# Optimization experiments

Hardware: AMD Instinct MI355X
Metric: run time of the kernel (lower is better)

Reference implementation:

```python
import jax, jax.numpy as jnp
import numpy as np
from jax import lax

EPS = 1e-5

def _conv1d(x, w, b):
    # x: [B,C,L], w: [O,I,K], valid padding, stride 1
    y = lax.conv_general_dilated(x, w, window_strides=(1,), padding='VALID',
                                 dimension_numbers=('NCH', 'OIH', 'NCH'))
    return y + b[None, :, None]

def setup_inputs() -> dict:
    key = jax.random.key(0)
    ks = jax.random.split(key, 7)
    B, L, C = 16, 4096, 512
    x = jax.random.normal(ks[0], (B, L, C), dtype=jnp.float32)
    fan3 = 1.0 / np.sqrt(C * 3)
    fan1 = 1.0 / np.sqrt(C * 1)
    w_down = jax.random.uniform(ks[1], (C, C, 3), jnp.float32, -fan3, fan3)
    b_down = jax.random.uniform(ks[2], (C,), jnp.float32, -fan3, fan3)
    w_pad = jax.random.uniform(ks[3], (C, C, 1), jnp.float32, -fan1, fan1)
    b_pad = jax.random.uniform(ks[4], (C,), jnp.float32, -fan1, fan1)
    gamma = jnp.ones((C,), jnp.float32)
    beta = jnp.zeros((C,), jnp.float32)
    return {"x": x, "w_down": w_down, "b_down": b_down,
            "w_pad": w_pad, "b_pad": b_pad, "gamma": gamma, "beta": beta}

def reference(x, w_down, b_down, w_pad, b_pad, gamma, beta):
    # d == 2 branch of ConvLayer
    B, L, C = x.shape

    def branch(xs):  # xs: [B, L//2, C]
        xt = jnp.transpose(xs, (0, 2, 1))                 # [B,C,L/2]
        p1 = _conv1d(xt, w_down, b_down)                  # [B,C,L/2-2]
        p2 = _conv1d(xt[:, :, :2], w_pad, b_pad)          # [B,C,2]
        return jnp.concatenate([p1, p2], axis=2)          # [B,C,L/2]

    x1_p = branch(x[:, 0::2, :])
    x2_p = branch(x[:, 1::2, :])
    # interleave: even positions from x1_p, odd from x2_p
    x_p = jnp.stack([x1_p, x2_p], axis=3).reshape(B, C, L)

    # BatchNorm1d in training mode: batch stats over (batch, length)
    mean = jnp.mean(x_p, axis=(0, 2), keepdims=True)
    var = jnp.var(x_p, axis=(0, 2), keepdims=True)
    xn = (x_p - mean) * lax.rsqrt(var + EPS)
    xn = xn * gamma[None, :, None] + beta[None, :, None]

    y = jax.nn.elu(xn)                                    # dropout = identity (eval)
    y = y + jnp.transpose(x, (0, 2, 1))                   # residual [B,C,L]

    # MaxPool1d(kernel=3, stride=2, padding=1)
    yp = jnp.pad(y, ((0, 0), (0, 0), (1, 1)), constant_values=-jnp.inf)
    pooled = lax.reduce_window(yp, -jnp.inf, lax.max, (1, 1, 3), (1, 1, 2), 'VALID')
    return jnp.transpose(pooled, (0, 2, 1))               # [B, L//2, C]
```

## Files before the change

kernel.cpp:

```cpp
#include <hip/hip_runtime.h>
#include <hip/hip_bf16.h>
#include <math.h>

typedef __bf16 bf16;
typedef __bf16 bf16x8 __attribute__((ext_vector_type(8)));
typedef float floatx4 __attribute__((ext_vector_type(4)));

#define GAS __attribute__((address_space(1)))
#define LAS __attribute__((address_space(3)))

static constexpr int B_ = 16, L_ = 4096, C_ = 512;
static constexpr int M_ = B_ * L_;
static constexpr int K_ = 3 * C_;

__global__ void prep(const float* __restrict__ x, bf16* __restrict__ xb,
                     const float* __restrict__ wd, bf16* __restrict__ wr,
                     const float* __restrict__ wp, const float* __restrict__ bp,
                     bf16* __restrict__ xp, float* __restrict__ sums) {
    __shared__ float xrow[C_];
    if (blockIdx.x < 2048) {
        for (int u = blockIdx.x; u < 19456; u += 2048) {
            if (u < 16384) {
                const size_t i = ((size_t)u * 256 + threadIdx.x) * 8;
                floatx4 a = *(const floatx4*)(x + i);
                floatx4 b = *(const floatx4*)(x + i + 4);
                bf16x8 o;
#pragma unroll
                for (int j = 0; j < 4; ++j) { o[j] = (bf16)a[j]; o[4 + j] = (bf16)b[j]; }
                *(bf16x8*)(xb + i) = o;
            } else {
                int idx = (u - 16384) * 256 + threadIdx.x;
                int o   = idx / K_;
                int rem = idx - o * K_;
                int kk  = rem >> 9;
                int i   = rem & 511;
                wr[idx] = (bf16)wd[o * K_ + i * 3 + kk];
            }
        }
    } else {
        const int bid = blockIdx.x - 2048;
        const int b = bid >> 2;
        const int j = bid & 3;
        for (int i = threadIdx.x; i < C_; i += 256)
            xrow[i] = x[(size_t)(b * L_ + j) * C_ + i];
        __syncthreads();
        for (int c = threadIdx.x; c < C_; c += 256) {
            const float* w = wp + (size_t)c * C_;
            float acc = 0.f;
#pragma unroll 4
            for (int i = 0; i < C_; i += 4) {
                floatx4 wv = *(const floatx4*)(w + i);
#pragma unroll
                for (int u = 0; u < 4; ++u) acc += wv[u] * xrow[i + u];
            }
            const float v = acc + bp[c];
            xp[(size_t)(b * L_ + 4092 + j) * C_ + c] = (bf16)v;
            atomicAdd(&sums[c], v);
            atomicAdd(&sums[C_ + c], v * v);
        }
    }
}

__global__ __launch_bounds__(512, 2) void gemm_conv(
    const bf16* __restrict__ x, const bf16* __restrict__ wr,
    const float* __restrict__ bd, bf16* __restrict__ xp, float* __restrict__ sums)
{
    __shared__ bf16 As[2 * 256 * 64];
    __shared__ bf16 Bs[2 * 256 * 64];

    const int tid = threadIdx.x;
    const int u   = blockIdx.x;
    const int mb  = (u & 7) + 8 * (u >> 4);
    const int nb  = (u >> 3) & 1;
    const int m0  = mb * 256;
    const int n0  = nb * 256;

    const int wave = tid >> 6;
    const int lane = tid & 63;
    const int wm = wave & 1;
    const int wn = wave >> 1;
    const int tm = lane & 15;
    const int quad = lane >> 4;

    floatx4 acc[2][4][2][2];
#pragma unroll
    for (int a = 0; a < 2; ++a)
#pragma unroll
        for (int b = 0; b < 4; ++b)
#pragma unroll
            for (int c = 0; c < 2; ++c)
#pragma unroll
                for (int d = 0; d < 2; ++d) acc[a][b][c][d] = floatx4{0.f, 0.f, 0.f, 0.f};

    const int r0  = tid >> 3;
    const int c0s = (tid & 7) ^ (r0 & 7);

    auto stageA = [&](int t, int eta) {
        if (t >= 24) return;
        const int kk = t >> 3, i0 = (t & 7) << 6;
        bf16* dst = As + (t & 1) * 16384 + eta * 8192 + tid * 8;
        int sr0 = m0 + eta * 128 + r0 + 2 * kk;      if (sr0 > M_ - 1) sr0 = M_ - 1;
        int sr1 = m0 + eta * 128 + r0 + 64 + 2 * kk; if (sr1 > M_ - 1) sr1 = M_ - 1;
        __builtin_amdgcn_global_load_lds((const GAS void*)(x + (size_t)sr0 * C_ + i0 + c0s * 8),
                                         (LAS void*)dst, 16, 0, 0);
        __builtin_amdgcn_global_load_lds((const GAS void*)(x + (size_t)sr1 * C_ + i0 + c0s * 8),
                                         (LAS void*)(dst + 4096), 16, 0, 0);
    };
    auto stageB = [&](int t, int eta) {
        if (t >= 24) return;
        const int kk = t >> 3, i0 = (t & 7) << 6;
        bf16* dst = Bs + (t & 1) * 16384 + eta * 8192 + tid * 8;
        const bf16* s0 = wr + (size_t)(n0 + eta * 128 + r0) * K_ + kk * C_ + i0 + c0s * 8;
        __builtin_amdgcn_global_load_lds((const GAS void*)s0, (LAS void*)dst, 16, 0, 0);
        __builtin_amdgcn_global_load_lds((const GAS void*)(s0 + (size_t)64 * K_),
                                         (LAS void*)(dst + 4096), 16, 0, 0);
    };

    const int xo0 = (quad ^ (tm & 7)) << 3;
    const int xo1 = ((4 + quad) ^ (tm & 7)) << 3;

    bf16x8 af[4][2];
    bf16x8 bfr[2][2][2];

    stageA(0, 0); stageB(0, 0); stageB(0, 1); stageA(0, 1);
    stageA(1, 0); stageB(1, 0); stageB(1, 1); stageA(1, 1);
    asm volatile("s_waitcnt vmcnt(8)" ::: "memory");
    asm volatile("s_barrier" ::: "memory");
#pragma unroll
    for (int mi = 0; mi < 4; ++mi) {
        const bf16* p = As + (wm * 64 + mi * 16 + tm) * 64;
        af[mi][0] = *(const bf16x8*)(p + xo0);
        af[mi][1] = *(const bf16x8*)(p + xo1);
    }
#pragma unroll
    for (int ni = 0; ni < 2; ++ni) {
        const bf16* p = Bs + (wn * 32 + ni * 16 + tm) * 64;
        bfr[0][ni][0] = *(const bf16x8*)(p + xo0);
        bfr[0][ni][1] = *(const bf16x8*)(p + xo1);
    }

#pragma unroll 2
    for (int t = 0; t < 24; ++t) {
        const bf16* Ab  = As + (t & 1) * 16384;
        const bf16* Bb  = Bs + (t & 1) * 16384;
        const bf16* AbN = As + ((t + 1) & 1) * 16384;
        const bf16* BbN = Bs + ((t + 1) & 1) * 16384;

        asm volatile("s_waitcnt lgkmcnt(0)" ::: "memory");
        __builtin_amdgcn_sched_barrier(0);
        __builtin_amdgcn_s_setprio(1);
#pragma unroll
        for (int kh = 0; kh < 2; ++kh)
#pragma unroll
            for (int mi = 0; mi < 4; ++mi)
#pragma unroll
                for (int ni = 0; ni < 2; ++ni)
                    acc[0][mi][0][ni] = __builtin_amdgcn_mfma_f32_16x16x32_bf16(
                        af[mi][kh], bfr[0][ni][kh], acc[0][mi][0][ni], 0, 0, 0);
        __builtin_amdgcn_s_setprio(0);
#pragma unroll
        for (int ni = 0; ni < 2; ++ni) {
            const bf16* p = Bb + (128 + wn * 32 + ni * 16 + tm) * 64;
            bfr[1][ni][0] = *(const bf16x8*)(p + xo0);
            bfr[1][ni][1] = *(const bf16x8*)(p + xo1);
        }
        asm volatile("s_barrier" ::: "memory");

        asm volatile("s_waitcnt lgkmcnt(0)" ::: "memory");
        __builtin_amdgcn_sched_barrier(0);
        __builtin_amdgcn_s_setprio(1);
#pragma unroll
        for (int kh = 0; kh < 2; ++kh)
#pragma unroll
            for (int mi = 0; mi < 4; ++mi)
#pragma unroll
                for (int ni = 0; ni < 2; ++ni)
                    acc[0][mi][1][ni] = __builtin_amdgcn_mfma_f32_16x16x32_bf16(
                        af[mi][kh], bfr[1][ni][kh], acc[0][mi][1][ni], 0, 0, 0);
        __builtin_amdgcn_s_setprio(0);
#pragma unroll
        for (int mi = 0; mi < 4; ++mi) {
            const bf16* p = Ab + (128 + wm * 64 + mi * 16 + tm) * 64;
            af[mi][0] = *(const bf16x8*)(p + xo0);
            af[mi][1] = *(const bf16x8*)(p + xo1);
        }
        stageA(t + 2, 0);
        stageB(t + 2, 0);
        asm volatile("s_barrier" ::: "memory");

        asm volatile("s_waitcnt lgkmcnt(0)" ::: "memory");
        __builtin_amdgcn_sched_barrier(0);
        __builtin_amdgcn_s_setprio(1);
#pragma unroll
        for (int kh = 0; kh < 2; ++kh)
#pragma unroll
            for (int mi = 0; mi < 4; ++mi)
#pragma unroll
                for (int ni = 0; ni < 2; ++ni)
                    acc[1][mi][1][ni] = __builtin_amdgcn_mfma_f32_16x16x32_bf16(
                        af[mi][kh], bfr[1][ni][kh], acc[1][mi][1][ni], 0, 0, 0);
        __builtin_amdgcn_s_setprio(0);
        stageB(t + 2, 1);
        asm volatile("s_barrier" ::: "memory");

        stageA(t + 2, 1);
        if (t < 22)       { asm volatile("s_waitcnt vmcnt(8)" ::: "memory"); }
        else if (t == 22) { asm volatile("s_waitcnt vmcnt(0)" ::: "memory"); }
        asm volatile("s_barrier" ::: "memory");
        __builtin_amdgcn_s_setprio(1);
#pragma unroll
        for (int kh = 0; kh < 2; ++kh)
#pragma unroll
            for (int mi = 0; mi < 4; ++mi)
#pragma unroll
                for (int ni = 0; ni < 2; ++ni)
                    acc[1][mi][0][ni] = __builtin_amdgcn_mfma_f32_16x16x32_bf16(
                        af[mi][kh], bfr[0][ni][kh], acc[1][mi][0][ni], 0, 0, 0);
        __builtin_amdgcn_s_setprio(0);
        if (t < 23) {
#pragma unroll
            for (int mi = 0; mi < 4; ++mi) {
                const bf16* p = AbN + (wm * 64 + mi * 16 + tm) * 64;
                af[mi][0] = *(const bf16x8*)(p + xo0);
                af[mi][1] = *(const bf16x8*)(p + xo1);
            }
#pragma unroll
            for (int ni = 0; ni < 2; ++ni) {
                const bf16* p = BbN + (wn * 32 + ni * 16 + tm) * 64;
                bfr[0][ni][0] = *(const bf16x8*)(p + xo0);
                bfr[0][ni][1] = *(const bf16x8*)(p + xo1);
            }
        }
        asm volatile("s_barrier" ::: "memory");
    }

    float bias[2][2], s[2][2], q[2][2];
#pragma unroll
    for (int nh = 0; nh < 2; ++nh)
#pragma unroll
        for (int ni = 0; ni < 2; ++ni) {
            bias[nh][ni] = bd[n0 + nh * 128 + wn * 32 + ni * 16 + tm];
            s[nh][ni] = 0.f; q[nh][ni] = 0.f;
        }

#pragma unroll
    for (int mh = 0; mh < 2; ++mh)
#pragma unroll
        for (int mi = 0; mi < 4; ++mi)
#pragma unroll
            for (int r = 0; r < 4; ++r) {
                const int m = m0 + mh * 128 + wm * 64 + mi * 16 + quad * 4 + r;
                const bool valid = (m & (L_ - 1)) < L_ - 4;
                bf16* dst = xp + (size_t)m * C_ + n0 + wn * 32 + tm;
#pragma unroll
                for (int nh = 0; nh < 2; ++nh)
#pragma unroll
                    for (int ni = 0; ni < 2; ++ni) {
                        const float v = acc[mh][mi][nh][ni][r] + bias[nh][ni];
                        if (valid) {
                            dst[nh * 128 + ni * 16] = (bf16)v;
                            s[nh][ni] += v; q[nh][ni] += v * v;
                        }
                    }
            }
#pragma unroll
    for (int nh = 0; nh < 2; ++nh)
#pragma unroll
        for (int ni = 0; ni < 2; ++ni) {
            float sv = s[nh][ni], qv = q[nh][ni];
            sv += __shfl_xor(sv, 16); sv += __shfl_xor(sv, 32);
            qv += __shfl_xor(qv, 16); qv += __shfl_xor(qv, 32);
            if (quad == 0) {
                const int c = n0 + nh * 128 + wn * 32 + ni * 16 + tm;
                atomicAdd(&sums[c], sv);
                atomicAdd(&sums[C_ + c], qv);
            }
        }
}

__global__ void final_pool(const bf16* __restrict__ xp, const bf16* __restrict__ xb,
                           const float* __restrict__ sums, const float* __restrict__ gamma,
                           const float* __restrict__ beta, float* __restrict__ out)
{
    const int gid0 = blockIdx.x * 256 + threadIdx.x;
    const int cg = gid0 & 63;
    const int t  = (gid0 >> 6) & 2047;
    const int b0 = gid0 >> 17;
    const int c0 = cg << 3;

    float sc[8], sh[8];
    const float invn = 1.0f / 65536.0f;
#pragma unroll
    for (int j = 0; j < 8; ++j) {
        const int c = c0 + j;
        float mean = sums[c] * invn;
        float var  = sums[C_ + c] * invn - mean * mean;
        float scale = gamma[c] * rsqrtf(var + 1e-5f);
        sc[j] = scale;
        sh[j] = beta[c] - mean * scale;
    }

    for (int b = b0; b < B_; b += 4) {
        float best[8];
#pragma unroll
        for (int j = 0; j < 8; ++j) best[j] = -INFINITY;

#pragma unroll
        for (int dl = -1; dl <= 1; ++dl) {
            const int l = 2 * t + dl;
            if (l < 0) continue;
            const size_t off = (size_t)(b * L_ + l) * C_ + c0;
            bf16x8 xpv = *(const bf16x8*)(xp + off);
            bf16x8 xv  = *(const bf16x8*)(xb + off);
#pragma unroll
            for (int j = 0; j < 8; ++j) {
                float z = sc[j] * (float)xpv[j] + sh[j];
                float y = (z > 0.f) ? z : (__expf(z) - 1.f);
                y += (float)xv[j];
                best[j] = fmaxf(best[j], y);
            }
        }
        floatx4 o0, o1;
#pragma unroll
        for (int j = 0; j < 4; ++j) { o0[j] = best[j]; o1[j] = best[4 + j]; }
        const size_t og = ((size_t)b << 17) | ((size_t)t << 6) | cg;
        *(floatx4*)(out + og * 8) = o0;
        *(floatx4*)(out + og * 8 + 4) = o1;
    }
}

extern "C" void kernel_launch(void* const* d_in, const int* in_sizes, int n_in,
                              void* d_out, int out_size, void* d_ws, size_t ws_size,
                              hipStream_t stream)
{
    const float* x      = (const float*)d_in[0];
    const float* w_down = (const float*)d_in[1];
    const float* b_down = (const float*)d_in[2];
    const float* w_pad  = (const float*)d_in[3];
    const float* b_pad  = (const float*)d_in[4];
    const float* gamma  = (const float*)d_in[5];
    const float* beta   = (const float*)d_in[6];
    float* out = (float*)d_out;

    char* ws = (char*)d_ws;
    bf16*  xb   = (bf16*)ws;
    bf16*  xp   = (bf16*)(ws + (size_t)M_ * C_ * 2);
    bf16*  wr   = (bf16*)(ws + (size_t)M_ * C_ * 4);
    float* sums = (float*)(ws + (size_t)M_ * C_ * 4 + (size_t)C_ * K_ * 2);

    hipMemsetAsync(sums, 0, 2 * C_ * sizeof(float), stream);
    prep<<<dim3(2048 + 64), dim3(256), 0, stream>>>(x, xb, w_down, wr,
                                                    w_pad, b_pad, xp, sums);
    gemm_conv<<<dim3(512), dim3(512), 0, stream>>>(xb, wr, b_down, xp, sums);
    final_pool<<<dim3(2048), dim3(256), 0, stream>>>(xp, xb, sums, gamma, beta, out);
}
```

Baseline: 402.3 us.

## Fuse fp32-to-bf16 conversion of x into the GEMM A-tile staging

The standalone conversion pass that turned x into a bf16 copy is removed from the prep kernel. The GEMM now loads fp32 x straight into registers, converts it to bf16 and writes it to LDS itself. Blocks with nb==0 also write the bf16 tile out for the later pooling kernel, which avoids a separate full read/write pass over x. In exchange, each A load fetches twice the bytes (fp32), uses more registers, and gives up the async global_load_lds path for A, with changed vmcnt wait accounting.

```diff
diff --git a/kernel.cpp b/kernel.cpp
--- a/kernel.cpp
+++ b/kernel.cpp
@@ -13,32 +13,22 @@
 static constexpr int M_ = B_ * L_;
 static constexpr int K_ = 3 * C_;
 
-__global__ void prep(const float* __restrict__ x, bf16* __restrict__ xb,
-                     const float* __restrict__ wd, bf16* __restrict__ wr,
-                     const float* __restrict__ wp, const float* __restrict__ bp,
-                     bf16* __restrict__ xp, float* __restrict__ sums) {
+__global__ void prep_w(const float* __restrict__ x,
+                       const float* __restrict__ wd, bf16* __restrict__ wr,
+                       const float* __restrict__ wp, const float* __restrict__ bp,
+                       bf16* __restrict__ xp, float* __restrict__ sums) {
     __shared__ float xrow[C_];
-    if (blockIdx.x < 2048) {
-        for (int u = blockIdx.x; u < 19456; u += 2048) {
-            if (u < 16384) {
-                const size_t i = ((size_t)u * 256 + threadIdx.x) * 8;
-                floatx4 a = *(const floatx4*)(x + i);
-                floatx4 b = *(const floatx4*)(x + i + 4);
-                bf16x8 o;
-#pragma unroll
-                for (int j = 0; j < 4; ++j) { o[j] = (bf16)a[j]; o[4 + j] = (bf16)b[j]; }
-                *(bf16x8*)(xb + i) = o;
-            } else {
-                int idx = (u - 16384) * 256 + threadIdx.x;
-                int o   = idx / K_;
-                int rem = idx - o * K_;
-                int kk  = rem >> 9;
-                int i   = rem & 511;
-                wr[idx] = (bf16)wd[o * K_ + i * 3 + kk];
-            }
+    if (blockIdx.x < 512) {
+        for (int u = blockIdx.x; u < 3072; u += 512) {
+            int idx = u * 256 + threadIdx.x;
+            int o   = idx / K_;
+            int rem = idx - o * K_;
+            int kk  = rem >> 9;
+            int i   = rem & 511;
+            wr[idx] = (bf16)wd[o * K_ + i * 3 + kk];
         }
     } else {
-        const int bid = blockIdx.x - 2048;
+        const int bid = blockIdx.x - 512;
         const int b = bid >> 2;
         const int j = bid & 3;
         for (int i = threadIdx.x; i < C_; i += 256)
@@ -62,8 +52,9 @@
 }
 
 __global__ __launch_bounds__(512, 2) void gemm_conv(
-    const bf16* __restrict__ x, const bf16* __restrict__ wr,
-    const float* __restrict__ bd, bf16* __restrict__ xp, float* __restrict__ sums)
+    const float* __restrict__ xf, const bf16* __restrict__ wr,
+    const float* __restrict__ bd, bf16* __restrict__ xp,
+    bf16* __restrict__ xb, float* __restrict__ sums)
 {
     __shared__ bf16 As[2 * 256 * 64];
     __shared__ bf16 Bs[2 * 256 * 64];
@@ -95,16 +86,41 @@
     const int r0  = tid >> 3;
     const int c0s = (tid & 7) ^ (r0 & 7);
 
-    auto stageA = [&](int t, int eta) {
-        if (t >= 24) return;
-        const int kk = t >> 3, i0 = (t & 7) << 6;
-        bf16* dst = As + (t & 1) * 16384 + eta * 8192 + tid * 8;
-        int sr0 = m0 + eta * 128 + r0 + 2 * kk;      if (sr0 > M_ - 1) sr0 = M_ - 1;
-        int sr1 = m0 + eta * 128 + r0 + 64 + 2 * kk; if (sr1 > M_ - 1) sr1 = M_ - 1;
-        __builtin_amdgcn_global_load_lds((const GAS void*)(x + (size_t)sr0 * C_ + i0 + c0s * 8),
-                                         (LAS void*)dst, 16, 0, 0);
-        __builtin_amdgcn_global_load_lds((const GAS void*)(x + (size_t)sr1 * C_ + i0 + c0s * 8),
-                                         (LAS void*)(dst + 4096), 16, 0, 0);
+    auto issueA = [&](int ts, floatx4 (&va)[8]) {
+        if (ts >= 24) return;
+        const int kk = ts >> 3, i0 = (ts & 7) << 6;
+#pragma unroll
+        for (int eta = 0; eta < 2; ++eta) {
+            int sr0 = m0 + eta * 128 + r0 + 2 * kk;      if (sr0 > M_ - 1) sr0 = M_ - 1;
+            int sr1 = m0 + eta * 128 + r0 + 64 + 2 * kk; if (sr1 > M_ - 1) sr1 = M_ - 1;
+            const float* p0 = xf + (size_t)sr0 * C_ + i0 + c0s * 8;
+            const float* p1 = xf + (size_t)sr1 * C_ + i0 + c0s * 8;
+            va[eta * 4 + 0] = *(const floatx4*)(p0);
+            va[eta * 4 + 1] = *(const floatx4*)(p0 + 4);
+            va[eta * 4 + 2] = *(const floatx4*)(p1);
+            va[eta * 4 + 3] = *(const floatx4*)(p1 + 4);
+        }
+    };
+    auto writeA = [&](int ts, const floatx4 (&va)[8]) {
+        if (ts >= 24) return;
+#pragma unroll
+        for (int eta = 0; eta < 2; ++eta) {
+            bf16* dst = As + (ts & 1) * 16384 + eta * 8192 + tid * 8;
+            bf16x8 v0, v1;
+#pragma unroll
+            for (int j = 0; j < 4; ++j) {
+                v0[j] = (bf16)va[eta * 4 + 0][j]; v0[4 + j] = (bf16)va[eta * 4 + 1][j];
+                v1[j] = (bf16)va[eta * 4 + 2][j]; v1[4 + j] = (bf16)va[eta * 4 + 3][j];
+            }
+            *(bf16x8*)dst = v0;
+            *(bf16x8*)(dst + 4096) = v1;
+            if (nb == 0 && ts < 8) {
+                const int i0 = ts << 6;
+                const int sr0 = m0 + eta * 128 + r0;
+                *(bf16x8*)(xb + (size_t)sr0 * C_ + i0 + c0s * 8) = v0;
+                *(bf16x8*)(xb + (size_t)(sr0 + 64) * C_ + i0 + c0s * 8) = v1;
+            }
+        }
     };
     auto stageB = [&](int t, int eta) {
         if (t >= 24) return;
@@ -122,10 +138,17 @@
     bf16x8 af[4][2];
     bf16x8 bfr[2][2][2];
 
-    stageA(0, 0); stageB(0, 0); stageB(0, 1); stageA(0, 1);
-    stageA(1, 0); stageB(1, 0); stageB(1, 1); stageA(1, 1);
-    asm volatile("s_waitcnt vmcnt(8)" ::: "memory");
-    asm volatile("s_barrier" ::: "memory");
+    {
+        floatx4 va0[8], va1[8];
+        issueA(0, va0);
+        issueA(1, va1);
+        stageB(0, 0); stageB(0, 1); stageB(1, 0); stageB(1, 1);
+        asm volatile("s_waitcnt vmcnt(8)" ::: "memory");
+        writeA(0, va0);
+        writeA(1, va1);
+        asm volatile("s_waitcnt vmcnt(12) lgkmcnt(0)" ::: "memory");
+        asm volatile("s_barrier" ::: "memory");
+    }
 #pragma unroll
     for (int mi = 0; mi < 4; ++mi) {
         const bf16* p = As + (wm * 64 + mi * 16 + tm) * 64;
@@ -145,6 +168,7 @@
         const bf16* Bb  = Bs + (t & 1) * 16384;
         const bf16* AbN = As + ((t + 1) & 1) * 16384;
         const bf16* BbN = Bs + ((t + 1) & 1) * 16384;
+        floatx4 va[8];
 
         asm volatile("s_waitcnt lgkmcnt(0)" ::: "memory");
         __builtin_amdgcn_sched_barrier(0);
@@ -184,7 +208,7 @@
             af[mi][0] = *(const bf16x8*)(p + xo0);
             af[mi][1] = *(const bf16x8*)(p + xo1);
         }
-        stageA(t + 2, 0);
+        issueA(t + 2, va);
         stageB(t + 2, 0);
         asm volatile("s_barrier" ::: "memory");
 
@@ -203,9 +227,9 @@
         stageB(t + 2, 1);
         asm volatile("s_barrier" ::: "memory");
 
-        stageA(t + 2, 1);
-        if (t < 22)       { asm volatile("s_waitcnt vmcnt(8)" ::: "memory"); }
+        if (t < 22)       { asm volatile("s_waitcnt vmcnt(4)" ::: "memory"); }
         else if (t == 22) { asm volatile("s_waitcnt vmcnt(0)" ::: "memory"); }
+        writeA(t + 2, va);
         asm volatile("s_barrier" ::: "memory");
         __builtin_amdgcn_s_setprio(1);
 #pragma unroll
@@ -349,8 +373,8 @@
     float* sums = (float*)(ws + (size_t)M_ * C_ * 4 + (size_t)C_ * K_ * 2);
 
     hipMemsetAsync(sums, 0, 2 * C_ * sizeof(float), stream);
-    prep<<<dim3(2048 + 64), dim3(256), 0, stream>>>(x, xb, w_down, wr,
-                                                    w_pad, b_pad, xp, sums);
-    gemm_conv<<<dim3(512), dim3(512), 0, stream>>>(xb, wr, b_down, xp, sums);
+    prep_w<<<dim3(512 + 64), dim3(256), 0, stream>>>(x, w_down, wr,
+                                                     w_pad, b_pad, xp, sums);
+    gemm_conv<<<dim3(512), dim3(512), 0, stream>>>(x, wr, b_down, xp, xb, sums);
     final_pool<<<dim3(2048), dim3(256), 0, stream>>>(xp, xb, sums, gamma, beta, out);
 }
```

Result: slower. 418.0 us (+3.9%).
